# Kernel tuning notes

Measured on AMD Instinct MI355X. Metric: run time of the kernel, lower is better.

## Reference

```python
import jax, jax.numpy as jnp
import numpy as np


def setup_inputs() -> dict:
    key = jax.random.key(0)
    k1, k2 = jax.random.split(key)
    B, S, H, E = 8, 4096, 16, 64
    s = int(S ** 0.5)  # 64
    v = jax.random.normal(k1, (B, S, H, E), dtype=jnp.float32)
    w = jax.random.normal(k2, (1, H, 2 * s - 1), dtype=jnp.float32)  # 'full' bias base
    o_ = jnp.ones((s,), dtype=jnp.float32)
    return {"v": v, "w": w, "o_": o_}


def reference(v, w, o_):
    # FFTBias2d forward, bias_base_type='full', has_specials=False.
    B, S, H, E = v.shape
    s = int(S ** 0.5)  # grid side; S == s*s

    # z = w[..., shape_-seq_len : shape_+seq_len-1] with seq_len==shape_ -> whole w (len 2s-1)
    z = w[..., s - s : s + s - 1]          # (1, H, 2s-1)
    z_fft = jnp.fft.rfft(z)                # (1, H, s)

    # [B,S,H,E] -> [B,E,H,S] -> [B,E,H,s,s] -> [B,E,s,H,s]
    v_ = jnp.transpose(v, (0, 3, 2, 1)).reshape(B, E, H, s, s)
    v_ = jnp.transpose(v_, (0, 1, 3, 2, 4))

    # row-sum path: sum over first grid axis -> [B,E,H,s]
    v_s = v_.sum(-3)
    v_m = jnp.pad(v_s, ((0, 0), (0, 0), (0, 0), (s - 1, 0)))  # len 2s-1
    v_m_fft = jnp.fft.rfft(v_m)

    # col-sum path: [B,E,s2,H,s1] summed over s2 -> [B,E,H,s]
    u_s = jnp.transpose(v_, (0, 1, 4, 3, 2)).sum(-3)
    u_m = jnp.pad(u_s, ((0, 0), (0, 0), (0, 0), (s - 1, 0)))
    u_m_fft = jnp.fft.rfft(u_m)

    zf = jnp.expand_dims(z_fft, axis=1)    # (1, 1, H, s) broadcasts vs (B, E, H, s)
    RxV_m = jnp.fft.irfft(v_m_fft * zf)[..., :s]  # (B, E, H, s)
    RxU_m = jnp.fft.irfft(u_m_fft * zf)[..., :s]

    # outer sum over the two grid axes -> (B, E, H, s, s) -> (B, S, H, E)
    pbv = RxV_m[..., None, :] + RxU_m[..., :, None]
    pbv = pbv.reshape(B, E, H, S)
    pbv = jnp.transpose(pbv, (0, 3, 2, 1))

    # normalizer path
    o_pad = jnp.pad(o_, (s - 1, 0))        # len 2s-1
    o_fft = jnp.fft.rfft(o_pad)            # (s,)
    z_pb = jnp.fft.irfft(o_fft * z_fft)[..., :s] * s  # (1, H, s)
    z_pb = z_pb[..., None, :] + z_pb[..., :, None]    # (1, H, s, s)
    z_pb = z_pb.reshape(-1, H, S)
    z_pb = jnp.transpose(z_pb, (0, 2, 1))  # (1, S, H)
    return pbv, z_pb
```

## Files before the change

### kernel.cpp

```cpp
#include <hip/hip_runtime.h>
#include <stdint.h>

#define OUT2_OFF 33554432ull

typedef float v4f __attribute__((ext_vector_type(4)));

__device__ __forceinline__ v4f shflx4(v4f s, int m) {
    v4f r;
    r.x = __shfl_xor(s.x, m);
    r.y = __shfl_xor(s.y, m);
    r.z = __shfl_xor(s.z, m);
    r.w = __shfl_xor(s.w, m);
    return r;
}

__global__ __launch_bounds__(256) void fused1_kernel(
        const float* __restrict__ v,
        const float* __restrict__ wgt,
        float* __restrict__ us,
        float* __restrict__ vs_part,
        float* __restrict__ G) {
    const int bid = blockIdx.x;
    const int tid = threadIdx.x;

    __shared__ __align__(16) v4f upart[4][16][16];
    __shared__ float zl[127];
    __shared__ float c127t[127], s127t[127];
    __shared__ float c126t[126], s126t[126];
    __shared__ float ZA[64], ZB[64];

    if (bid < 512) {
        const int ig = bid & 3, bh = bid >> 2;
        const int b = bh >> 4, h = bh & 15;
        const int g = tid >> 4;
        const int q = tid & 15;
        const int w = tid >> 6;
        const int lane = tid & 63;
        const int s1 = (lane >> 4) & 1, s2 = (lane >> 5) & 1;

        const v4f* v4 = (const v4f*)v;
        const size_t baseq =
            (size_t)b * 1048576 + (size_t)(ig * 1024 + g) * 256 + h * 16 + q;

        v4f vsacc[4], uacc[8], buf[8];
#pragma unroll
        for (int a = 0; a < 4; ++a) vsacc[a] = (v4f)0.f;
#pragma unroll
        for (int a = 0; a < 8; ++a) uacc[a] = (v4f)0.f;

#pragma unroll
        for (int k0 = 0; k0 < 8; ++k0)
            buf[k0] = __builtin_nontemporal_load(v4 + baseq + (size_t)k0 * 4096);

#pragma unroll
        for (int k = 0; k < 64; ++k) {
            v4f c = buf[k & 7];
            if (k < 56)
                buf[k & 7] = __builtin_nontemporal_load(
                    v4 + baseq + (size_t)(k + 8) * 4096);
            vsacc[k & 3] += c;
            uacc[(k >> 2) & 7] += c;
            if ((k & 31) == 31) {
                const int h0 = k >> 5;
                v4f t4[4];
#pragma unroll
                for (int m = 0; m < 4; ++m) {
                    v4f keep = s1 ? uacc[m + 4] : uacc[m];
                    v4f send = s1 ? uacc[m] : uacc[m + 4];
                    t4[m] = keep + shflx4(send, 16);
                }
#pragma unroll
                for (int m = 0; m < 2; ++m) {
                    v4f keep = s2 ? t4[m + 2] : t4[m];
                    v4f send = s2 ? t4[m] : t4[m + 2];
                    v4f r = keep + shflx4(send, 32);
                    upart[w][h0 * 8 + m + 2 * s2 + 4 * s1][q] = r;
                }
#pragma unroll
                for (int m = 0; m < 8; ++m) uacc[m] = (v4f)0.f;
            }
        }
#pragma unroll
        for (int jh = 0; jh < 4; ++jh)
            *(v4f*)(vs_part + (((size_t)ig * 128 + bh) * 64 + g + 16 * jh) * 64 +
                    q * 4) = vsacc[jh];
        __syncthreads();
        {
            const int i = tid >> 4, q2 = tid & 15;
            v4f ssum = (upart[0][i][q2] + upart[1][i][q2]) +
                       (upart[2][i][q2] + upart[3][i][q2]);
            *(v4f*)(us + ((size_t)bh * 64 + ig * 16 + i) * 64 + q2 * 4) = ssum;
        }
    } else {
        const int pb = bid - 512;
        const int h = pb >> 4, tq = pb & 15;
        const float w127 = 6.28318530717958647692f / 127.0f;
        const float w126 = 6.28318530717958647692f / 126.0f;
        if (tid < 127) {
            zl[tid] = wgt[h * 127 + tid];
            float sv, cv; __sincosf((float)tid * w127, &sv, &cv);
            c127t[tid] = cv; s127t[tid] = sv;
        } else if (tid >= 128 && tid < 254) {
            const int m = tid - 128;
            float sv, cv; __sincosf((float)m * w126, &sv, &cv);
            c126t[m] = cv; s126t[m] = sv;
        }
        __syncthreads();
        if (tid < 64) {
            const int k = tid;
            float a = 0.f, bq = 0.f;
            int r = 0;
            for (int m = 0; m < 127; ++m) {
                a  += zl[m] * c127t[r];
                bq -= zl[m] * s127t[r];
                r += k; if (r >= 127) r -= 127;
            }
            ZA[k] = a; ZB[k] = bq;
        }
        __syncthreads();
        const int t = tq * 4 + (tid >> 6);
        const int j = tid & 63;
        const int jj = 63 + j;
        float acc = ZA[0];
        int rb = t, ra = jj;
        for (int k = 1; k <= 62; ++k) {
            const float cA = c126t[rb], sA = s126t[rb];
            const float cB = c127t[ra], sB = s127t[ra];
            const float cAB = cA * cB + sA * sB;
            const float sAB = sA * cB - cA * sB;
            acc += 2.f * (ZA[k] * cAB - ZB[k] * sAB);
            rb += t;  if (rb >= 126) rb -= 126;
            ra += jj; if (ra >= 127) ra -= 127;
        }
        {
            const int rn = (63 * jj) % 127;
            const float term = ZA[63] * c127t[rn] + ZB[63] * s127t[rn];
            acc += (t & 1) ? -term : term;
        }
        G[((size_t)h * 64 + t) * 64 + j] = acc * (1.0f / 126.0f);
    }
}

union K2Smem {
    struct { float GlT[64 * 68]; float usl[4096]; float vsl[4096]; } a;
    struct { float rxv[64 * 68]; float rxu[16 * 68]; } p2;
    struct { float zpb[1024]; float ol[64]; } t;
};

__global__ __launch_bounds__(256) void convemit_kernel(
        const float* __restrict__ G,
        const float* __restrict__ us,
        const float* __restrict__ vs_part,
        const float* __restrict__ ovec,
        float* __restrict__ out) {
    const int bid = blockIdx.x;
    const int tid = threadIdx.x;

    __shared__ __align__(16) K2Smem sm;

    if (bid < 512) {
        const int bh = bid >> 2, tq = bid & 3;
        const int b = bh >> 4, h = bh & 15;

        const v4f* usg = (const v4f*)(us + (size_t)bh * 4096);
        const v4f* vp0 = (const v4f*)(vs_part + (size_t)bh * 4096);
        const v4f* vp1 = (const v4f*)(vs_part + (size_t)(128 + bh) * 4096);
        const v4f* vp2 = (const v4f*)(vs_part + (size_t)(256 + bh) * 4096);
        const v4f* vp3 = (const v4f*)(vs_part + (size_t)(384 + bh) * 4096);
        const v4f* Gg  = (const v4f*)(G + (size_t)h * 4096);

#pragma unroll
        for (int k = 0; k < 4; ++k) {
            const int vi = k * 256 + tid;
            const int fi = vi * 4;
            v4f uu = usg[vi];
            *(v4f*)&sm.a.usl[fi] = uu;
            v4f a = (vp0[vi] + vp1[vi]) + (vp2[vi] + vp3[vi]);
            *(v4f*)&sm.a.vsl[fi] = a;
            v4f g = Gg[vi];
            const int t = fi >> 6, j0 = fi & 63;
            sm.a.GlT[(j0 + 0) * 68 + t] = g.x;
            sm.a.GlT[(j0 + 1) * 68 + t] = g.y;
            sm.a.GlT[(j0 + 2) * 68 + t] = g.z;
            sm.a.GlT[(j0 + 3) * 68 + t] = g.w;
        }
        __syncthreads();

        const int tb = tid >> 4;
        const int q  = tid & 15;
        const int i_row = tq * 16 + tb;
        v4f accV[4];
#pragma unroll
        for (int r = 0; r < 4; ++r) accV[r] = (v4f)0.f;
        v4f accU = (v4f)0.f;
        {
            const v4f* us4 = (const v4f*)sm.a.usl;
            const v4f* vs4 = (const v4f*)sm.a.vsl;
#pragma unroll 8
            for (int j = 0; j < 64; ++j) {
                const v4f gv = *(const v4f*)&sm.a.GlT[j * 68 + tb * 4];
                const float gu = sm.a.GlT[j * 68 + i_row];
                const v4f vv = vs4[j * 16 + q];
                const v4f uu = us4[j * 16 + q];
                accV[0] += gv.x * vv;
                accV[1] += gv.y * vv;
                accV[2] += gv.z * vv;
                accV[3] += gv.w * vv;
                accU += gu * uu;
            }
        }
        __syncthreads();
#pragma unroll
        for (int r = 0; r < 4; ++r)
            *(v4f*)&sm.p2.rxv[(tb * 4 + r) * 68 + q * 4] = accV[r];
        *(v4f*)&sm.p2.rxu[tb * 68 + q * 4] = accU;
        __syncthreads();

        const int w = tid >> 6, lane = tid & 63;
        const int jsub = lane >> 4, qq = lane & 15;
        v4f rv4[4];
#pragma unroll
        for (int jj = 0; jj < 4; ++jj)
            rv4[jj] = *(const v4f*)&sm.p2.rxv[(jj * 16 + w * 4 + jsub) * 68 + qq * 4];
        const size_t obase =
            (((size_t)b * 4096 + tq * 1024) * 16 + h) * 64 + qq * 4;
        for (int il = 0; il < 16; ++il) {
            const v4f ru = *(const v4f*)&sm.p2.rxu[il * 68 + qq * 4];
#pragma unroll
            for (int jj = 0; jj < 4; ++jj) {
                const int j = jj * 16 + w * 4 + jsub;
                __builtin_nontemporal_store(rv4[jj] + ru,
                    (v4f*)(out + obase + (size_t)(il * 64 + j) * 1024));
            }
        }
    } else {
        const int bz = bid - 512;
        if (tid < 64) sm.t.ol[tid] = ovec[tid];
        __syncthreads();
#pragma unroll
        for (int r = 0; r < 4; ++r) {
            const int idx = tid + 256 * r;
            const int h = idx >> 6, n = idx & 63;
            const v4f* G4 = (const v4f*)(G + (size_t)h * 4096 + n * 64);
            v4f acc4 = (v4f)0.f;
#pragma unroll
            for (int jv = 0; jv < 16; ++jv)
                acc4 += (*(const v4f*)&sm.t.ol[jv * 4]) * G4[jv];
            sm.t.zpb[idx] = (acc4.x + acc4.y + acc4.z + acc4.w) * 64.f;
        }
        __syncthreads();
#pragma unroll
        for (int r = 0; r < 4; ++r) {
            const int k = tid + 256 * r;
            const int hh = k & 15, c = k >> 4;
            out[OUT2_OFF + ((size_t)(bz * 64 + c)) * 16 + hh] =
                sm.t.zpb[hh * 64 + c] + sm.t.zpb[hh * 64 + bz];
        }
    }
}

extern "C" void kernel_launch(void* const* d_in, const int* in_sizes, int n_in,
                              void* d_out, int out_size, void* d_ws, size_t ws_size,
                              hipStream_t stream) {
    const float* v    = (const float*)d_in[0];
    const float* wgt  = (const float*)d_in[1];
    const float* ovec = (const float*)d_in[2];

    float* G       = (float*)d_ws;
    float* us      = G + 65536;
    float* vs_part = us + 524288;
    float* out     = (float*)d_out;

    hipLaunchKernelGGL(fused1_kernel,   dim3(512 + 256), dim3(256), 0, stream,
                       v, wgt, us, vs_part, G);
    hipLaunchKernelGGL(convemit_kernel, dim3(512 + 64),  dim3(256), 0, stream,
                       G, us, vs_part, ovec, out);
}
```

Measured before the change: 240.9 us.

## Fuse both kernels into one cooperative kernel with per-head atomic flag dependencies

Replaces the two-kernel sequence with a single cooperative launch of 512 blocks. Blocks first do the bias-FFT work (blocks 256+) and the reduction work, then signal completion through atomic counters in workspace. Dependent conv/emit phases spin-wait on those counters instead of waiting at a kernel boundary. The goal is to remove the launch gap and let phases overlap. In exchange it adds a memset, spin-wait overhead and a union-sized shared allocation, and it falls back to the old two-kernel path when workspace is too small or the cooperative launch fails.

```diff
diff --git a/kernel.cpp b/kernel.cpp
--- a/kernel.cpp
+++ b/kernel.cpp
@@ -2,6 +2,7 @@
 #include <stdint.h>
 
 #define OUT2_OFF 33554432ull
+#define WS_DATA_BYTES 10747904ull
 
 typedef float v4f __attribute__((ext_vector_type(4)));
 
@@ -14,22 +15,84 @@
     return r;
 }
 
-__global__ __launch_bounds__(256) void fused1_kernel(
+union Smem {
+    struct { v4f upart[4][16][16]; } r;
+    struct {
+        float zl[127], c127[127], s127[127];
+        float c126[126], s126[126], ZA[64], ZB[64];
+    } p;
+    struct { float GlT[64 * 68]; float usl[4096]; float vsl[4096]; } a;
+    struct { float rxv[64 * 68]; float rxu[16 * 68]; } p2;
+    struct { float zpb[1024]; float ol[64]; } t;
+};
+
+__global__ __launch_bounds__(256, 2) void mega_kernel(
         const float* __restrict__ v,
         const float* __restrict__ wgt,
         float* __restrict__ us,
         float* __restrict__ vs_part,
-        float* __restrict__ G) {
+        float* __restrict__ G,
+        const float* __restrict__ ovec,
+        float* __restrict__ out,
+        unsigned* __restrict__ flags) {
     const int bid = blockIdx.x;
     const int tid = threadIdx.x;
 
-    __shared__ __align__(16) v4f upart[4][16][16];
-    __shared__ float zl[127];
-    __shared__ float c127t[127], s127t[127];
-    __shared__ float c126t[126], s126t[126];
-    __shared__ float ZA[64], ZB[64];
-
-    if (bid < 512) {
+    __shared__ __align__(16) Smem sm;
+
+    if (bid >= 256) {
+        const int pb = bid - 256;
+        const int h = pb >> 4, tq = pb & 15;
+        const float w127 = 6.28318530717958647692f / 127.0f;
+        const float w126 = 6.28318530717958647692f / 126.0f;
+        if (tid < 127) {
+            sm.p.zl[tid] = wgt[h * 127 + tid];
+            float sv, cv; __sincosf((float)tid * w127, &sv, &cv);
+            sm.p.c127[tid] = cv; sm.p.s127[tid] = sv;
+        } else if (tid >= 128 && tid < 254) {
+            const int m = tid - 128;
+            float sv, cv; __sincosf((float)m * w126, &sv, &cv);
+            sm.p.c126[m] = cv; sm.p.s126[m] = sv;
+        }
+        __syncthreads();
+        if (tid < 64) {
+            const int k = tid;
+            float a = 0.f, bq = 0.f;
+            int r = 0;
+            for (int m = 0; m < 127; ++m) {
+                a  += sm.p.zl[m] * sm.p.c127[r];
+                bq -= sm.p.zl[m] * sm.p.s127[r];
+                r += k; if (r >= 127) r -= 127;
+            }
+            sm.p.ZA[k] = a; sm.p.ZB[k] = bq;
+        }
+        __syncthreads();
+        {
+            const int t = tq * 4 + (tid >> 6);
+            const int j = tid & 63;
+            const int jj = 63 + j;
+            float acc = sm.p.ZA[0];
+            int rb = t, ra = jj;
+            for (int k = 1; k <= 62; ++k) {
+                const float cA = sm.p.c126[rb], sA = sm.p.s126[rb];
+                const float cB = sm.p.c127[ra], sB = sm.p.s127[ra];
+                const float cAB = cA * cB + sA * sB;
+                const float sAB = sA * cB - cA * sB;
+                acc += 2.f * (sm.p.ZA[k] * cAB - sm.p.ZB[k] * sAB);
+                rb += t;  if (rb >= 126) rb -= 126;
+                ra += jj; if (ra >= 127) ra -= 127;
+            }
+            const int rn = (63 * jj) % 127;
+            const float term =
+                sm.p.ZA[63] * sm.p.c127[rn] + sm.p.ZB[63] * sm.p.s127[rn];
+            acc += (t & 1) ? -term : term;
+            G[((size_t)h * 64 + t) * 64 + j] = acc * (1.0f / 126.0f);
+        }
+        __syncthreads();
+        if (tid == 0) { __threadfence(); atomicAdd(&flags[128 + h], 1u); }
+    }
+
+    {
         const int ig = bid & 3, bh = bid >> 2;
         const int b = bh >> 4, h = bh & 15;
         const int g = tid >> 4;
@@ -74,7 +137,7 @@
                     v4f keep = s2 ? t4[m + 2] : t4[m];
                     v4f send = s2 ? t4[m] : t4[m + 2];
                     v4f r = keep + shflx4(send, 32);
-                    upart[w][h0 * 8 + m + 2 * s2 + 4 * s1][q] = r;
+                    sm.r.upart[w][h0 * 8 + m + 2 * s2 + 4 * s1][q] = r;
                 }
 #pragma unroll
                 for (int m = 0; m < 8; ++m) uacc[m] = (v4f)0.f;
@@ -87,80 +150,25 @@
         __syncthreads();
         {
             const int i = tid >> 4, q2 = tid & 15;
-            v4f ssum = (upart[0][i][q2] + upart[1][i][q2]) +
-                       (upart[2][i][q2] + upart[3][i][q2]);
+            v4f ssum = (sm.r.upart[0][i][q2] + sm.r.upart[1][i][q2]) +
+                       (sm.r.upart[2][i][q2] + sm.r.upart[3][i][q2]);
             *(v4f*)(us + ((size_t)bh * 64 + ig * 16 + i) * 64 + q2 * 4) = ssum;
         }
-    } else {
-        const int pb = bid - 512;
-        const int h = pb >> 4, tq = pb & 15;
-        const float w127 = 6.28318530717958647692f / 127.0f;
-        const float w126 = 6.28318530717958647692f / 126.0f;
-        if (tid < 127) {
-            zl[tid] = wgt[h * 127 + tid];
-            float sv, cv; __sincosf((float)tid * w127, &sv, &cv);
-            c127t[tid] = cv; s127t[tid] = sv;
-        } else if (tid >= 128 && tid < 254) {
-            const int m = tid - 128;
-            float sv, cv; __sincosf((float)m * w126, &sv, &cv);
-            c126t[m] = cv; s126t[m] = sv;
-        }
-        __syncthreads();
-        if (tid < 64) {
-            const int k = tid;
-            float a = 0.f, bq = 0.f;
-            int r = 0;
-            for (int m = 0; m < 127; ++m) {
-                a  += zl[m] * c127t[r];
-                bq -= zl[m] * s127t[r];
-                r += k; if (r >= 127) r -= 127;
-            }
-            ZA[k] = a; ZB[k] = bq;
-        }
-        __syncthreads();
-        const int t = tq * 4 + (tid >> 6);
-        const int j = tid & 63;
-        const int jj = 63 + j;
-        float acc = ZA[0];
-        int rb = t, ra = jj;
-        for (int k = 1; k <= 62; ++k) {
-            const float cA = c126t[rb], sA = s126t[rb];
-            const float cB = c127t[ra], sB = s127t[ra];
-            const float cAB = cA * cB + sA * sB;
-            const float sAB = sA * cB - cA * sB;
-            acc += 2.f * (ZA[k] * cAB - ZB[k] * sAB);
-            rb += t;  if (rb >= 126) rb -= 126;
-            ra += jj; if (ra >= 127) ra -= 127;
-        }
-        {
-            const int rn = (63 * jj) % 127;
-            const float term = ZA[63] * c127t[rn] + ZB[63] * s127t[rn];
-            acc += (t & 1) ? -term : term;
-        }
-        G[((size_t)h * 64 + t) * 64 + j] = acc * (1.0f / 126.0f);
-    }
-}
-
-union K2Smem {
-    struct { float GlT[64 * 68]; float usl[4096]; float vsl[4096]; } a;
-    struct { float rxv[64 * 68]; float rxu[16 * 68]; } p2;
-    struct { float zpb[1024]; float ol[64]; } t;
-};
-
-__global__ __launch_bounds__(256) void convemit_kernel(
-        const float* __restrict__ G,
-        const float* __restrict__ us,
-        const float* __restrict__ vs_part,
-        const float* __restrict__ ovec,
-        float* __restrict__ out) {
-    const int bid = blockIdx.x;
-    const int tid = threadIdx.x;
-
-    __shared__ __align__(16) K2Smem sm;
-
-    if (bid < 512) {
+        __syncthreads();
+        if (tid == 0) { __threadfence(); atomicAdd(&flags[bh], 1u); }
+    }
+
+    {
         const int bh = bid >> 2, tq = bid & 3;
         const int b = bh >> 4, h = bh & 15;
+
+        if (tid == 0) {
+            while (atomicAdd(&flags[bh], 0u) < 4u) __builtin_amdgcn_s_sleep(2);
+            while (atomicAdd(&flags[128 + h], 0u) < 16u)
+                __builtin_amdgcn_s_sleep(2);
+            __threadfence();
+        }
+        __syncthreads();
 
         const v4f* usg = (const v4f*)(us + (size_t)bh * 4096);
         const v4f* vp0 = (const v4f*)(vs_part + (size_t)bh * 4096);
@@ -233,6 +241,260 @@
                     (v4f*)(out + obase + (size_t)(il * 64 + j) * 1024));
             }
         }
+    }
+
+    if (bid < 64) {
+        const int bz = bid;
+        if (tid == 0) {
+            for (int hh = 0; hh < 16; ++hh)
+                while (atomicAdd(&flags[128 + hh], 0u) < 16u)
+                    __builtin_amdgcn_s_sleep(2);
+            __threadfence();
+        }
+        __syncthreads();
+        if (tid < 64) sm.t.ol[tid] = ovec[tid];
+        __syncthreads();
+#pragma unroll
+        for (int r = 0; r < 4; ++r) {
+            const int idx = tid + 256 * r;
+            const int h = idx >> 6, n = idx & 63;
+            const v4f* G4 = (const v4f*)(G + (size_t)h * 4096 + n * 64);
+            v4f acc4 = (v4f)0.f;
+#pragma unroll
+            for (int jv = 0; jv < 16; ++jv)
+                acc4 += (*(const v4f*)&sm.t.ol[jv * 4]) * G4[jv];
+            sm.t.zpb[idx] = (acc4.x + acc4.y + acc4.z + acc4.w) * 64.f;
+        }
+        __syncthreads();
+#pragma unroll
+        for (int r = 0; r < 4; ++r) {
+            const int k = tid + 256 * r;
+            const int hh = k & 15, c = k >> 4;
+            out[OUT2_OFF + ((size_t)(bz * 64 + c)) * 16 + hh] =
+                sm.t.zpb[hh * 64 + c] + sm.t.zpb[hh * 64 + bz];
+        }
+    }
+}
+
+__global__ __launch_bounds__(256) void fused1_kernel(
+        const float* __restrict__ v,
+        const float* __restrict__ wgt,
+        float* __restrict__ us,
+        float* __restrict__ vs_part,
+        float* __restrict__ G) {
+    const int bid = blockIdx.x;
+    const int tid = threadIdx.x;
+
+    __shared__ __align__(16) v4f upart[4][16][16];
+    __shared__ float zl[127];
+    __shared__ float c127t[127], s127t[127];
+    __shared__ float c126t[126], s126t[126];
+    __shared__ float ZA[64], ZB[64];
+
+    if (bid < 512) {
+        const int ig = bid & 3, bh = bid >> 2;
+        const int b = bh >> 4, h = bh & 15;
+        const int g = tid >> 4;
+        const int q = tid & 15;
+        const int w = tid >> 6;
+        const int lane = tid & 63;
+        const int s1 = (lane >> 4) & 1, s2 = (lane >> 5) & 1;
+
+        const v4f* v4 = (const v4f*)v;
+        const size_t baseq =
+            (size_t)b * 1048576 + (size_t)(ig * 1024 + g) * 256 + h * 16 + q;
+
+        v4f vsacc[4], uacc[8], buf[8];
+#pragma unroll
+        for (int a = 0; a < 4; ++a) vsacc[a] = (v4f)0.f;
+#pragma unroll
+        for (int a = 0; a < 8; ++a) uacc[a] = (v4f)0.f;
+
+#pragma unroll
+        for (int k0 = 0; k0 < 8; ++k0)
+            buf[k0] = __builtin_nontemporal_load(v4 + baseq + (size_t)k0 * 4096);
+
+#pragma unroll
+        for (int k = 0; k < 64; ++k) {
+            v4f c = buf[k & 7];
+            if (k < 56)
+                buf[k & 7] = __builtin_nontemporal_load(
+                    v4 + baseq + (size_t)(k + 8) * 4096);
+            vsacc[k & 3] += c;
+            uacc[(k >> 2) & 7] += c;
+            if ((k & 31) == 31) {
+                const int h0 = k >> 5;
+                v4f t4[4];
+#pragma unroll
+                for (int m = 0; m < 4; ++m) {
+                    v4f keep = s1 ? uacc[m + 4] : uacc[m];
+                    v4f send = s1 ? uacc[m] : uacc[m + 4];
+                    t4[m] = keep + shflx4(send, 16);
+                }
+#pragma unroll
+                for (int m = 0; m < 2; ++m) {
+                    v4f keep = s2 ? t4[m + 2] : t4[m];
+                    v4f send = s2 ? t4[m] : t4[m + 2];
+                    v4f r = keep + shflx4(send, 32);
+                    upart[w][h0 * 8 + m + 2 * s2 + 4 * s1][q] = r;
+                }
+#pragma unroll
+                for (int m = 0; m < 8; ++m) uacc[m] = (v4f)0.f;
+            }
+        }
+#pragma unroll
+        for (int jh = 0; jh < 4; ++jh)
+            *(v4f*)(vs_part + (((size_t)ig * 128 + bh) * 64 + g + 16 * jh) * 64 +
+                    q * 4) = vsacc[jh];
+        __syncthreads();
+        {
+            const int i = tid >> 4, q2 = tid & 15;
+            v4f ssum = (upart[0][i][q2] + upart[1][i][q2]) +
+                       (upart[2][i][q2] + upart[3][i][q2]);
+            *(v4f*)(us + ((size_t)bh * 64 + ig * 16 + i) * 64 + q2 * 4) = ssum;
+        }
+    } else {
+        const int pb = bid - 512;
+        const int h = pb >> 4, tq = pb & 15;
+        const float w127 = 6.28318530717958647692f / 127.0f;
+        const float w126 = 6.28318530717958647692f / 126.0f;
+        if (tid < 127) {
+            zl[tid] = wgt[h * 127 + tid];
+            float sv, cv; __sincosf((float)tid * w127, &sv, &cv);
+            c127t[tid] = cv; s127t[tid] = sv;
+        } else if (tid >= 128 && tid < 254) {
+            const int m = tid - 128;
+            float sv, cv; __sincosf((float)m * w126, &sv, &cv);
+            c126t[m] = cv; s126t[m] = sv;
+        }
+        __syncthreads();
+        if (tid < 64) {
+            const int k = tid;
+            float a = 0.f, bq = 0.f;
+            int r = 0;
+            for (int m = 0; m < 127; ++m) {
+                a  += zl[m] * c127t[r];
+                bq -= zl[m] * s127t[r];
+                r += k; if (r >= 127) r -= 127;
+            }
+            ZA[k] = a; ZB[k] = bq;
+        }
+        __syncthreads();
+        const int t = tq * 4 + (tid >> 6);
+        const int j = tid & 63;
+        const int jj = 63 + j;
+        float acc = ZA[0];
+        int rb = t, ra = jj;
+        for (int k = 1; k <= 62; ++k) {
+            const float cA = c126t[rb], sA = s126t[rb];
+            const float cB = c127t[ra], sB = s127t[ra];
+            const float cAB = cA * cB + sA * sB;
+            const float sAB = sA * cB - cA * sB;
+            acc += 2.f * (ZA[k] * cAB - ZB[k] * sAB);
+            rb += t;  if (rb >= 126) rb -= 126;
+            ra += jj; if (ra >= 127) ra -= 127;
+        }
+        {
+            const int rn = (63 * jj) % 127;
+            const float term = ZA[63] * c127t[rn] + ZB[63] * s127t[rn];
+            acc += (t & 1) ? -term : term;
+        }
+        G[((size_t)h * 64 + t) * 64 + j] = acc * (1.0f / 126.0f);
+    }
+}
+
+union K2Smem {
+    struct { float GlT[64 * 68]; float usl[4096]; float vsl[4096]; } a;
+    struct { float rxv[64 * 68]; float rxu[16 * 68]; } p2;
+    struct { float zpb[1024]; float ol[64]; } t;
+};
+
+__global__ __launch_bounds__(256) void convemit_kernel(
+        const float* __restrict__ G,
+        const float* __restrict__ us,
+        const float* __restrict__ vs_part,
+        const float* __restrict__ ovec,
+        float* __restrict__ out) {
+    const int bid = blockIdx.x;
+    const int tid = threadIdx.x;
+
+    __shared__ __align__(16) K2Smem sm;
+
+    if (bid < 512) {
+        const int bh = bid >> 2, tq = bid & 3;
+        const int b = bh >> 4, h = bh & 15;
+
+        const v4f* usg = (const v4f*)(us + (size_t)bh * 4096);
+        const v4f* vp0 = (const v4f*)(vs_part + (size_t)bh * 4096);
+        const v4f* vp1 = (const v4f*)(vs_part + (size_t)(128 + bh) * 4096);
+        const v4f* vp2 = (const v4f*)(vs_part + (size_t)(256 + bh) * 4096);
+        const v4f* vp3 = (const v4f*)(vs_part + (size_t)(384 + bh) * 4096);
+        const v4f* Gg  = (const v4f*)(G + (size_t)h * 4096);
+
+#pragma unroll
+        for (int k = 0; k < 4; ++k) {
+            const int vi = k * 256 + tid;
+            const int fi = vi * 4;
+            v4f uu = usg[vi];
+            *(v4f*)&sm.a.usl[fi] = uu;
+            v4f a = (vp0[vi] + vp1[vi]) + (vp2[vi] + vp3[vi]);
+            *(v4f*)&sm.a.vsl[fi] = a;
+            v4f g = Gg[vi];
+            const int t = fi >> 6, j0 = fi & 63;
+            sm.a.GlT[(j0 + 0) * 68 + t] = g.x;
+            sm.a.GlT[(j0 + 1) * 68 + t] = g.y;
+            sm.a.GlT[(j0 + 2) * 68 + t] = g.z;
+            sm.a.GlT[(j0 + 3) * 68 + t] = g.w;
+        }
+        __syncthreads();
+
+        const int tb = tid >> 4;
+        const int q  = tid & 15;
+        const int i_row = tq * 16 + tb;
+        v4f accV[4];
+#pragma unroll
+        for (int r = 0; r < 4; ++r) accV[r] = (v4f)0.f;
+        v4f accU = (v4f)0.f;
+        {
+            const v4f* us4 = (const v4f*)sm.a.usl;
+            const v4f* vs4 = (const v4f*)sm.a.vsl;
+#pragma unroll 8
+            for (int j = 0; j < 64; ++j) {
+                const v4f gv = *(const v4f*)&sm.a.GlT[j * 68 + tb * 4];
+                const float gu = sm.a.GlT[j * 68 + i_row];
+                const v4f vv = vs4[j * 16 + q];
+                const v4f uu = us4[j * 16 + q];
+                accV[0] += gv.x * vv;
+                accV[1] += gv.y * vv;
+                accV[2] += gv.z * vv;
+                accV[3] += gv.w * vv;
+                accU += gu * uu;
+            }
+        }
+        __syncthreads();
+#pragma unroll
+        for (int r = 0; r < 4; ++r)
+            *(v4f*)&sm.p2.rxv[(tb * 4 + r) * 68 + q * 4] = accV[r];
+        *(v4f*)&sm.p2.rxu[tb * 68 + q * 4] = accU;
+        __syncthreads();
+
+        const int w = tid >> 6, lane = tid & 63;
+        const int jsub = lane >> 4, qq = lane & 15;
+        v4f rv4[4];
+#pragma unroll
+        for (int jj = 0; jj < 4; ++jj)
+            rv4[jj] = *(const v4f*)&sm.p2.rxv[(jj * 16 + w * 4 + jsub) * 68 + qq * 4];
+        const size_t obase =
+            (((size_t)b * 4096 + tq * 1024) * 16 + h) * 64 + qq * 4;
+        for (int il = 0; il < 16; ++il) {
+            const v4f ru = *(const v4f*)&sm.p2.rxu[il * 68 + qq * 4];
+#pragma unroll
+            for (int jj = 0; jj < 4; ++jj) {
+                const int j = jj * 16 + w * 4 + jsub;
+                __builtin_nontemporal_store(rv4[jj] + ru,
+                    (v4f*)(out + obase + (size_t)(il * 64 + j) * 1024));
+            }
+        }
     } else {
         const int bz = bid - 512;
         if (tid < 64) sm.t.ol[tid] = ovec[tid];
@@ -271,8 +533,19 @@
     float* vs_part = us + 524288;
     float* out     = (float*)d_out;
 
-    hipLaunchKernelGGL(fused1_kernel,   dim3(512 + 256), dim3(256), 0, stream,
-                       v, wgt, us, vs_part, G);
-    hipLaunchKernelGGL(convemit_kernel, dim3(512 + 64),  dim3(256), 0, stream,
-                       G, us, vs_part, ovec, out);
+    hipError_t err = hipErrorUnknown;
+    if (ws_size >= WS_DATA_BYTES + 4096ull) {
+        unsigned* flags = (unsigned*)((char*)d_ws + (ws_size - 4096));
+        hipMemsetAsync(flags, 0, 1024, stream);
+        void* args[] = {(void*)&v, (void*)&wgt, (void*)&us, (void*)&vs_part,
+                        (void*)&G, (void*)&ovec, (void*)&out, (void*)&flags};
+        err = hipLaunchCooperativeKernel((const void*)mega_kernel, dim3(512),
+                                         dim3(256), args, 0, stream);
+    }
+    if (err != hipSuccess) {
+        hipLaunchKernelGGL(fused1_kernel,   dim3(512 + 256), dim3(256), 0, stream,
+                           v, wgt, us, vs_part, G);
+        hipLaunchKernelGGL(convemit_kernel, dim3(512 + 64),  dim3(256), 0, stream,
+                           G, us, vs_part, ovec, out);
+    }
 }
```

Result: slower. 324.4 us (+34.7%).
